# Optimization experiments

Measured on AMD Instinct MI355X. Metric: run time of the kernel, lower is better.

The kernel has to match this reference:

```python
import jax, jax.numpy as jnp
import numpy as np

WINDOW_SIZE = 5
CONSISTENCY_WEIGHT = 1.0


def _wsum(x, w):
    # sliding-window sum along axis 1 via exclusive cumsum differences
    s = jnp.cumsum(x, axis=1)
    s = jnp.pad(s, ((0, 0), (1, 0)))
    return s[:, w:] - s[:, :-w]  # [B, L-w+1]


def setup_inputs() -> dict:
    key = jax.random.key(0)
    k1, k2, k3 = jax.random.split(key, 3)
    B, L, C = 512, 16384, 2
    return {
        "predictions": jax.random.normal(k1, (B, L, C), dtype=jnp.float32),
        "targets": jax.random.randint(k2, (B, L), 0, 2, dtype=jnp.int32),
        "mask": jax.random.randint(k3, (B, L), 0, 2, dtype=jnp.int32),
    }


def reference(predictions, targets, mask):
    w = WINDOW_SIZE
    probs = jax.nn.softmax(predictions, axis=-1)[..., 1]  # [B, L]
    t = targets.astype(jnp.float32)
    m = mask.astype(jnp.float32)

    msum = _wsum(m, w)                       # [B, W]
    denom = jnp.maximum(msum, 1.0)           # clamp(min=1.0)
    spm = _wsum(probs * m, w)
    stm = _wsum(t * m, w)
    sp2m = _wsum(probs * probs * m, w)
    st2m = _wsum(t * t * m, w)

    pmean = spm / denom
    tmean = stm / denom
    # masked biased variance: sum((x - mean)^2 * m) / clamp(msum, 1)
    pvar = (sp2m - 2.0 * pmean * spm + pmean * pmean * msum) / denom
    tvar = (st2m - 2.0 * tmean * stm + tmean * tmean * msum) / denom

    mse = jnp.mean((pvar - tvar) ** 2, axis=0)          # per-window MSE over batch, [W]
    valid = (jnp.sum(msum, axis=0) > 0).astype(jnp.float32)  # skip windows with zero mask
    cnt = jnp.maximum(jnp.sum(valid), 1.0)
    loss = jnp.sum(mse * valid) / cnt * CONSISTENCY_WEIGHT
    return loss
```

## Files before the change

kernel.cpp:

```cpp
#include <hip/hip_runtime.h>
#include <math.h>

#define BATCH 512
#define LEN   16384
#define WIN   5
#define WOUT  (LEN - WIN + 1)
#define TPB   256
#define WPT   4
#define WPB   (TPB * WPT)
#define EPT   (WPT + WIN - 1)
#define NCH2  8

__device__ __forceinline__ float fast_rcp(float x) {
    float r = __builtin_amdgcn_rcpf(x);
    return r * fmaf(-x, r, 2.0f);
}

struct Row {
    int4   m0, m1, t0, t1;
    float4 q0, q1, q2, q3;
};

__device__ __forceinline__ Row load_row(const float* __restrict__ pred,
                                        const int*   __restrict__ tgt,
                                        const int*   __restrict__ msk,
                                        size_t base) {
    Row r;
    r.m0 = *(const int4*)(msk + base);
    r.m1 = *(const int4*)(msk + base + 4);
    r.t0 = *(const int4*)(tgt + base);
    r.t1 = *(const int4*)(tgt + base + 4);
    r.q0 = *(const float4*)(pred + base * 2);
    r.q1 = *(const float4*)(pred + base * 2 + 4);
    r.q2 = *(const float4*)(pred + base * 2 + 8);
    r.q3 = *(const float4*)(pred + base * 2 + 12);
    return r;
}

__device__ __forceinline__ void accum_row(const Row& r,
                                          float accd2[WPT], float accms[WPT]) {
    float m[EPT], tm[EPT], pm[EPT], p2m[EPT];
    {
        const int mi[EPT] = {r.m0.x, r.m0.y, r.m0.z, r.m0.w,
                             r.m1.x, r.m1.y, r.m1.z, r.m1.w};
        const int ti[EPT] = {r.t0.x, r.t0.y, r.t0.z, r.t0.w,
                             r.t1.x, r.t1.y, r.t1.z, r.t1.w};
        const float dx[EPT] = {r.q0.x - r.q0.y, r.q0.z - r.q0.w,
                               r.q1.x - r.q1.y, r.q1.z - r.q1.w,
                               r.q2.x - r.q2.y, r.q2.z - r.q2.w,
                               r.q3.x - r.q3.y, r.q3.z - r.q3.w};
#pragma unroll
        for (int i = 0; i < EPT; ++i) {
            const float p  = fast_rcp(1.0f + __expf(dx[i]));
            const float mf = (float)mi[i];
            m[i]   = mf;
            tm[i]  = (float)(ti[i] & mi[i]);
            pm[i]  = p * mf;
            p2m[i] = p * p * mf;
        }
    }
#pragma unroll
    for (int w = 0; w < WPT; ++w) {
        float msum = 0.f, stm = 0.f, spm = 0.f, sp2m = 0.f;
#pragma unroll
        for (int k = 0; k < WIN; ++k) {
            msum += m[w + k];
            stm  += tm[w + k];
            spm  += pm[w + k];
            sp2m += p2m[w + k];
        }
        const float denom = fmaxf(msum, 1.0f);
        const float inv   = fast_rcp(denom);
        const float pmean = spm * inv;
        const float tmean = stm * inv;
        const float pvar  = (sp2m - 2.0f * pmean * spm + pmean * pmean * msum) * inv;
        const float tvar  = (stm  - 2.0f * tmean * stm + tmean * tmean * msum) * inv;
        const float d = pvar - tvar;
        accd2[w] += d * d;
        accms[w] += msum;
    }
}

__global__ __launch_bounds__(TPB, 4)
void bcl_partial_kernel(const float* __restrict__ pred,
                        const int*   __restrict__ tgt,
                        const int*   __restrict__ msk,
                        float* __restrict__ part_d2,
                        float* __restrict__ part_ms,
                        int bper) {
    const int j0 = blockIdx.x * WPB + (int)threadIdx.x * WPT;
    if (j0 >= WOUT) return;
    const int b0 = blockIdx.y * bper;

    float accd2[WPT] = {0.f, 0.f, 0.f, 0.f};
    float accms[WPT] = {0.f, 0.f, 0.f, 0.f};

    size_t base = (size_t)b0 * LEN + j0;

    Row A = load_row(pred, tgt, msk, base);

    for (int it = 0; it + 2 < bper; it += 2) {
        Row B = load_row(pred, tgt, msk, base + LEN);
        accum_row(A, accd2, accms);
        A = load_row(pred, tgt, msk, base + 2 * (size_t)LEN);
        accum_row(B, accd2, accms);
        base += 2 * (size_t)LEN;
    }
    {
        Row B = load_row(pred, tgt, msk, base + LEN);
        accum_row(A, accd2, accms);
        accum_row(B, accd2, accms);
    }

    *(float4*)(part_d2 + (size_t)blockIdx.y * WOUT + j0) =
        make_float4(accd2[0], accd2[1], accd2[2], accd2[3]);
    *(float4*)(part_ms + (size_t)blockIdx.y * WOUT + j0) =
        make_float4(accms[0], accms[1], accms[2], accms[3]);
}

__global__ __launch_bounds__(TPB)
void bcl_chunk_reduce(const float* __restrict__ part_d2,
                      const float* __restrict__ part_ms,
                      float* __restrict__ p2_d2,
                      float* __restrict__ p2_ms,
                      double* __restrict__ accum,
                      unsigned int* __restrict__ ticket,
                      int rf) {
    if (blockIdx.x == 0 && blockIdx.y == 0 && threadIdx.x == 0) {
        accum[0] = 0.0; accum[1] = 0.0; *ticket = 0u;
    }
    const int j = blockIdx.x * blockDim.x + threadIdx.x;
    if (j >= WOUT) return;
    const int c0 = blockIdx.y * rf;
    float d2 = 0.f, ms = 0.f;
#pragma unroll 8
    for (int c = c0; c < c0 + rf; ++c) {
        d2 += part_d2[(size_t)c * WOUT + j];
        ms += part_ms[(size_t)c * WOUT + j];
    }
    p2_d2[(size_t)blockIdx.y * WOUT + j] = d2;
    p2_ms[(size_t)blockIdx.y * WOUT + j] = ms;
}

__global__ __launch_bounds__(TPB)
void bcl_window_reduce(const float* __restrict__ p2_d2,
                       const float* __restrict__ p2_ms,
                       double* __restrict__ accum,
                       unsigned int* __restrict__ ticket,
                       float* __restrict__ out,
                       int nch2) {
    const int j = blockIdx.x * blockDim.x + threadIdx.x;
    double num = 0.0, cnt = 0.0;
    if (j < WOUT) {
        float d2 = 0.f, ms = 0.f;
#pragma unroll 8
        for (int c = 0; c < nch2; ++c) {
            d2 += p2_d2[(size_t)c * WOUT + j];
            ms += p2_ms[(size_t)c * WOUT + j];
        }
        if (ms > 0.f) {
            num = (double)d2 * (1.0 / (double)BATCH);
            cnt = 1.0;
        }
    }
    for (int off = 32; off > 0; off >>= 1) {
        num += __shfl_down(num, off, 64);
        cnt += __shfl_down(cnt, off, 64);
    }
    __shared__ double s_num[4], s_cnt[4];
    const int lane = threadIdx.x & 63, wave = threadIdx.x >> 6;
    if (lane == 0) { s_num[wave] = num; s_cnt[wave] = cnt; }
    __syncthreads();
    if (threadIdx.x == 0) {
        double n = 0.0, c = 0.0;
        const int nw = (int)(blockDim.x >> 6);
        for (int wv = 0; wv < nw; ++wv) { n += s_num[wv]; c += s_cnt[wv]; }
        atomicAdd(&accum[0], n);
        atomicAdd(&accum[1], c);
        __threadfence();
        const unsigned int t = atomicAdd(ticket, 1u);
        if (t == gridDim.x - 1) {
            out[0] = (float)(accum[0] / fmax(accum[1], 1.0));
        }
    }
}

extern "C" void kernel_launch(void* const* d_in, const int* in_sizes, int n_in,
                              void* d_out, int out_size, void* d_ws, size_t ws_size,
                              hipStream_t stream) {
    const float* pred = (const float*)d_in[0];
    const int*   tgt  = (const int*)d_in[1];
    const int*   msk  = (const int*)d_in[2];
    float* out = (float*)d_out;

    int nchunks = 64;
    while (nchunks > 2) {
        size_t need = (size_t)(nchunks + NCH2) * WOUT * 2 * sizeof(float) + 256;
        if (need <= ws_size) break;
        nchunks >>= 1;
    }
    const int bper = BATCH / nchunks;
    const int nch2 = (nchunks >= NCH2) ? NCH2 : nchunks;
    const int rf   = nchunks / nch2;

    float* part_d2 = (float*)d_ws;
    float* part_ms = part_d2 + (size_t)nchunks * WOUT;
    float* p2_d2   = part_ms + (size_t)nchunks * WOUT;
    float* p2_ms   = p2_d2   + (size_t)NCH2 * WOUT;
    size_t off = ((size_t)((char*)(p2_ms + (size_t)NCH2 * WOUT) - (char*)d_ws) + 15) & ~(size_t)15;
    double* accum = (double*)((char*)d_ws + off);
    unsigned int* ticket = (unsigned int*)(accum + 2);

    const int WBLKS = (WOUT + WPB - 1) / WPB;
    dim3 g1(WBLKS, nchunks);
    bcl_partial_kernel<<<g1, TPB, 0, stream>>>(pred, tgt, msk, part_d2, part_ms, bper);

    const int RBLKS = (WOUT + TPB - 1) / TPB;
    dim3 gA(RBLKS, nch2);
    bcl_chunk_reduce<<<gA, TPB, 0, stream>>>(part_d2, part_ms, p2_d2, p2_ms,
                                             accum, ticket, rf);

    bcl_window_reduce<<<RBLKS, TPB, 0, stream>>>(p2_d2, p2_ms, accum, ticket, out, nch2);
}
```

Measured before the change: 174.9 us.

## Software-pipeline row loads against window math and double the batch chunk count

Splits the per-row work into a convert stage and a window-reduction stage, and pipelines them so the next row's global loads are issued while the previous row's windows are computed. It drops the occupancy hint from the launch bounds, raises the batch chunk count from 64 to 128 for more blocks, and doubles the second-stage reduction width. The aim is to hide memory latency on a bandwidth-bound pass. In exchange it uses more registers and writes more partial-sum traffic to the workspace.

```diff
diff --git a/kernel.cpp b/kernel.cpp
--- a/kernel.cpp
+++ b/kernel.cpp
@@ -9,23 +9,27 @@
 #define WPT   4
 #define WPB   (TPB * WPT)
 #define EPT   (WPT + WIN - 1)
-#define NCH2  8
+#define NCH2  16
 
 __device__ __forceinline__ float fast_rcp(float x) {
     float r = __builtin_amdgcn_rcpf(x);
     return r * fmaf(-x, r, 2.0f);
 }
 
-struct Row {
+struct RowRaw {
     int4   m0, m1, t0, t1;
     float4 q0, q1, q2, q3;
 };
 
-__device__ __forceinline__ Row load_row(const float* __restrict__ pred,
-                                        const int*   __restrict__ tgt,
-                                        const int*   __restrict__ msk,
-                                        size_t base) {
-    Row r;
+struct RowArr {
+    float m[EPT], tm[EPT], pm[EPT], p2m[EPT];
+};
+
+__device__ __forceinline__ RowRaw load_row(const float* __restrict__ pred,
+                                           const int*   __restrict__ tgt,
+                                           const int*   __restrict__ msk,
+                                           size_t base) {
+    RowRaw r;
     r.m0 = *(const int4*)(msk + base);
     r.m1 = *(const int4*)(msk + base + 4);
     r.t0 = *(const int4*)(tgt + base);
@@ -37,37 +41,39 @@
     return r;
 }
 
-__device__ __forceinline__ void accum_row(const Row& r,
-                                          float accd2[WPT], float accms[WPT]) {
-    float m[EPT], tm[EPT], pm[EPT], p2m[EPT];
-    {
-        const int mi[EPT] = {r.m0.x, r.m0.y, r.m0.z, r.m0.w,
-                             r.m1.x, r.m1.y, r.m1.z, r.m1.w};
-        const int ti[EPT] = {r.t0.x, r.t0.y, r.t0.z, r.t0.w,
-                             r.t1.x, r.t1.y, r.t1.z, r.t1.w};
-        const float dx[EPT] = {r.q0.x - r.q0.y, r.q0.z - r.q0.w,
-                               r.q1.x - r.q1.y, r.q1.z - r.q1.w,
-                               r.q2.x - r.q2.y, r.q2.z - r.q2.w,
-                               r.q3.x - r.q3.y, r.q3.z - r.q3.w};
+__device__ __forceinline__ RowArr convert_row(const RowRaw& r) {
+    RowArr a;
+    const int mi[EPT] = {r.m0.x, r.m0.y, r.m0.z, r.m0.w,
+                         r.m1.x, r.m1.y, r.m1.z, r.m1.w};
+    const int ti[EPT] = {r.t0.x, r.t0.y, r.t0.z, r.t0.w,
+                         r.t1.x, r.t1.y, r.t1.z, r.t1.w};
+    const float dx[EPT] = {r.q0.x - r.q0.y, r.q0.z - r.q0.w,
+                           r.q1.x - r.q1.y, r.q1.z - r.q1.w,
+                           r.q2.x - r.q2.y, r.q2.z - r.q2.w,
+                           r.q3.x - r.q3.y, r.q3.z - r.q3.w};
 #pragma unroll
-        for (int i = 0; i < EPT; ++i) {
-            const float p  = fast_rcp(1.0f + __expf(dx[i]));
-            const float mf = (float)mi[i];
-            m[i]   = mf;
-            tm[i]  = (float)(ti[i] & mi[i]);
-            pm[i]  = p * mf;
-            p2m[i] = p * p * mf;
-        }
-    }
+    for (int i = 0; i < EPT; ++i) {
+        const float p  = fast_rcp(1.0f + __expf(dx[i]));
+        const float mf = (float)mi[i];
+        a.m[i]   = mf;
+        a.tm[i]  = (float)(ti[i] & mi[i]);
+        a.pm[i]  = p * mf;
+        a.p2m[i] = p * p * mf;
+    }
+    return a;
+}
+
+__device__ __forceinline__ void windows_row(const RowArr& a,
+                                            float accd2[WPT], float accms[WPT]) {
 #pragma unroll
     for (int w = 0; w < WPT; ++w) {
         float msum = 0.f, stm = 0.f, spm = 0.f, sp2m = 0.f;
 #pragma unroll
         for (int k = 0; k < WIN; ++k) {
-            msum += m[w + k];
-            stm  += tm[w + k];
-            spm  += pm[w + k];
-            sp2m += p2m[w + k];
+            msum += a.m[w + k];
+            stm  += a.tm[w + k];
+            spm  += a.pm[w + k];
+            sp2m += a.p2m[w + k];
         }
         const float denom = fmaxf(msum, 1.0f);
         const float inv   = fast_rcp(denom);
@@ -81,7 +87,7 @@
     }
 }
 
-__global__ __launch_bounds__(TPB, 4)
+__global__ __launch_bounds__(TPB)
 void bcl_partial_kernel(const float* __restrict__ pred,
                         const int*   __restrict__ tgt,
                         const int*   __restrict__ msk,
@@ -97,20 +103,15 @@
 
     size_t base = (size_t)b0 * LEN + j0;
 
-    Row A = load_row(pred, tgt, msk, base);
-
-    for (int it = 0; it + 2 < bper; it += 2) {
-        Row B = load_row(pred, tgt, msk, base + LEN);
-        accum_row(A, accd2, accms);
-        A = load_row(pred, tgt, msk, base + 2 * (size_t)LEN);
-        accum_row(B, accd2, accms);
-        base += 2 * (size_t)LEN;
-    }
-    {
-        Row B = load_row(pred, tgt, msk, base + LEN);
-        accum_row(A, accd2, accms);
-        accum_row(B, accd2, accms);
-    }
+    RowRaw raw = load_row(pred, tgt, msk, base);
+    RowArr arr = convert_row(raw);
+
+    for (int it = 1; it < bper; ++it) {
+        raw = load_row(pred, tgt, msk, base + (size_t)it * LEN);
+        windows_row(arr, accd2, accms);
+        arr = convert_row(raw);
+    }
+    windows_row(arr, accd2, accms);
 
     *(float4*)(part_d2 + (size_t)blockIdx.y * WOUT + j0) =
         make_float4(accd2[0], accd2[1], accd2[2], accd2[3]);
@@ -193,7 +194,7 @@
     const int*   msk  = (const int*)d_in[2];
     float* out = (float*)d_out;
 
-    int nchunks = 64;
+    int nchunks = 128;
     while (nchunks > 2) {
         size_t need = (size_t)(nchunks + NCH2) * WOUT * 2 * sizeof(float) + 256;
         if (need <= ws_size) break;
```

After: 164.7 us. 5.8% less time.
